# Kernel optimization log

Measured on AMD Instinct MI355X. Metric: run time of the kernel, lower is better.

Reference implementation:

```python
import jax, jax.numpy as jnp
import numpy as np

V = 100000   # vocab_size
E = 256      # embedding_dim
H = 256      # hidden_dim // 2 (per direction)
T = 32       # tagset_size
S = 4096     # seq_len
START, STOP = 30, 31
NEG = -10000.0


def setup_inputs() -> dict:
    key = jax.random.key(0)
    ks = jax.random.split(key, 13)
    sentence = jax.random.randint(ks[0], (S,), 0, V)
    h0 = jax.random.normal(ks[1], (2, H), dtype=jnp.float32)
    c0 = jax.random.normal(ks[2], (2, H), dtype=jnp.float32)
    embedding = jax.random.normal(ks[3], (V, E), dtype=jnp.float32) * 0.1
    # LSTM params, PyTorch layout: gates [i, f, g, o], combined bias = b_ih + b_hh
    w_ih_f = jax.random.normal(ks[4], (4 * H, E), dtype=jnp.float32) * 0.05
    w_hh_f = jax.random.normal(ks[5], (4 * H, H), dtype=jnp.float32) * 0.05
    b_f = jax.random.normal(ks[6], (4 * H,), dtype=jnp.float32) * 0.05
    w_ih_b = jax.random.normal(ks[7], (4 * H, E), dtype=jnp.float32) * 0.05
    w_hh_b = jax.random.normal(ks[8], (4 * H, H), dtype=jnp.float32) * 0.05
    b_b = jax.random.normal(ks[9], (4 * H,), dtype=jnp.float32) * 0.05
    lin_w = jax.random.normal(ks[10], (T, 2 * H), dtype=jnp.float32) * 0.05
    lin_b = jax.random.normal(ks[11], (T,), dtype=jnp.float32) * 0.05
    transitions = jax.random.normal(ks[12], (T, T), dtype=jnp.float32)
    transitions = transitions.at[START, :].set(NEG).at[:, STOP].set(NEG)
    return {"sentence": sentence, "h0": h0, "c0": c0, "embedding": embedding,
            "w_ih_f": w_ih_f, "w_hh_f": w_hh_f, "b_f": b_f,
            "w_ih_b": w_ih_b, "w_hh_b": w_hh_b, "b_b": b_b,
            "lin_w": lin_w, "lin_b": lin_b, "transitions": transitions}


def _lstm_dir(emb, h0, c0, w_ih, w_hh, b):
    # Precompute input contribution for all timesteps: [S, 4H]
    xg = emb @ w_ih.T + b

    def step(carry, xt):
        h, c = carry
        g = xt + h @ w_hh.T
        i, f, gg, o = jnp.split(g, 4)
        i = jax.nn.sigmoid(i); f = jax.nn.sigmoid(f)
        gg = jnp.tanh(gg); o = jax.nn.sigmoid(o)
        c = f * c + i * gg
        h = o * jnp.tanh(c)
        return (h, c), h

    _, hs = jax.lax.scan(step, (h0, c0), xg)
    return hs  # [S, H]


def reference(sentence, h0, c0, embedding, w_ih_f, w_hh_f, b_f,
              w_ih_b, w_hh_b, b_b, lin_w, lin_b, transitions):
    emb = embedding[sentence]                                    # [S, E]
    hs_f = _lstm_dir(emb, h0[0], c0[0], w_ih_f, w_hh_f, b_f)     # [S, H]
    hs_b = _lstm_dir(emb[::-1], h0[1], c0[1], w_ih_b, w_hh_b, b_b)[::-1]
    feats = jnp.concatenate([hs_f, hs_b], axis=-1) @ lin_w.T + lin_b  # [S, T]

    # Viterbi: forward_var over tags, vectorized over next/prev tags
    init = jnp.full((T,), NEG, dtype=feats.dtype).at[START].set(0.0)

    def vit_step(fv, feat):
        scores = fv[None, :] + transitions    # [next_tag, prev_tag]
        bp = jnp.argmax(scores, axis=1)       # best prev for each next tag
        fv_new = jnp.max(scores, axis=1) + feat
        return fv_new, bp

    fv, bps = jax.lax.scan(vit_step, init, feats)  # bps: [S, T]
    final = fv + transitions[STOP]
    last = jnp.argmax(final)
    score = final[last]

    # Backtrack (reverse scan); outputs[t] = best tag at timestep t
    def back_step(idx, bp):
        return bp[idx], idx

    _, path = jax.lax.scan(back_step, last, bps, reverse=True)
    return score, path
```

## Files before the change

### kernel.cpp

```cpp
#include <hip/hip_runtime.h>
#include <cstdint>
#include <cstddef>

#define S 4096
#define E 256
#define H 256
#define T 32
#define START_TAG 30
#define STOP_TAG 31
#define NEGV (-10000.0f)

typedef _Float16 half_t;
typedef _Float16 h2 __attribute__((ext_vector_type(2)));

__device__ __forceinline__ h2 f2h2(float a, float b) {
    h2 r; r[0] = (half_t)a; r[1] = (half_t)b; return r;
}
__device__ __forceinline__ h2 u2h2(unsigned int u) {
    h2 r; __builtin_memcpy(&r, &u, 4); return r;
}
__device__ __forceinline__ unsigned int h22u(h2 v) {
    unsigned int u; __builtin_memcpy(&u, &v, 4); return u;
}
__device__ __forceinline__ unsigned short f2h16(float f) {
    half_t h = (half_t)f;
    unsigned short u; __builtin_memcpy(&u, &h, 2); return u;
}
__device__ __forceinline__ float h16tof(unsigned short u) {
    half_t h; __builtin_memcpy(&h, &u, 2); return (float)h;
}

#if __has_builtin(__builtin_amdgcn_fdot2)
__device__ __forceinline__ float dot2(h2 a, h2 b, float c) {
    return __builtin_amdgcn_fdot2(a, b, c, false);
}
#else
__device__ __forceinline__ float dot2(h2 a, h2 b, float c) {
    return c + (float)a[0] * (float)b[0] + (float)a[1] * (float)b[1];
}
#endif

__device__ __forceinline__ float sigmoidf_(float x) {
    return 1.0f / (1.0f + __expf(-x));
}
__device__ __forceinline__ float tanhf_(float x) {
    return 1.0f - 2.0f / (__expf(2.0f * x) + 1.0f);
}

__device__ __forceinline__ float dpp_xor1_add(float x) {
    int yi = __builtin_amdgcn_update_dpp(0, __float_as_int(x), 0xB1, 0xF, 0xF, true);
    return x + __int_as_float(yi);
}

#define SBLK 16
__global__ __launch_bounds__(256) void xg_kernel(
    const int* __restrict__ sent, const float* __restrict__ emb,
    const float* __restrict__ w_ih_f, const float* __restrict__ b_f,
    const float* __restrict__ w_ih_b, const float* __restrict__ b_b,
    unsigned short* __restrict__ xg16s)
{
    const int dir = blockIdx.y;
    const int t0 = blockIdx.x * SBLK;
    const float* w_ih = dir ? w_ih_b : w_ih_f;
    const float* bias = dir ? b_b : b_f;

    __shared__ float embs[SBLK][E];
    for (int p = threadIdx.x; p < SBLK * (E / 4); p += 256) {
        int r = p >> 6, kq = p & 63;
        int t = t0 + r;
        int tt = dir ? (S - 1 - t) : t;
        int tok = sent[tt];
        float4 v = *(const float4*)(emb + (size_t)tok * E + 4 * kq);
        *(float4*)&embs[r][4 * kq] = v;
    }
    __syncthreads();

    for (int jj = 0; jj < 4; ++jj) {
        int j = jj * 256 + threadIdx.x;
        const float* wrow = w_ih + (size_t)j * E;
        float bv = bias[j];
        float acc[SBLK];
        #pragma unroll
        for (int t = 0; t < SBLK; ++t) acc[t] = bv;

        for (int kc = 0; kc < E / 16; ++kc) {
            float w[16];
            float4 a0 = *(const float4*)(wrow + kc * 16);
            float4 a1 = *(const float4*)(wrow + kc * 16 + 4);
            float4 a2 = *(const float4*)(wrow + kc * 16 + 8);
            float4 a3 = *(const float4*)(wrow + kc * 16 + 12);
            w[0] = a0.x; w[1] = a0.y; w[2] = a0.z; w[3] = a0.w;
            w[4] = a1.x; w[5] = a1.y; w[6] = a1.z; w[7] = a1.w;
            w[8] = a2.x; w[9] = a2.y; w[10] = a2.z; w[11] = a2.w;
            w[12] = a3.x; w[13] = a3.y; w[14] = a3.z; w[15] = a3.w;
            #pragma unroll
            for (int t = 0; t < SBLK; ++t) {
                const float* er = &embs[t][kc * 16];
                float s = 0.f;
                #pragma unroll
                for (int q = 0; q < 16; ++q) s += w[q] * er[q];
                acc[t] += s;
            }
        }
        const int u = threadIdx.x;
        #pragma unroll
        for (int t = 0; t < SBLK; ++t) {
            size_t base = (((size_t)dir * S + (size_t)(t0 + t)) * 256 + u) * 4 + jj;
            xg16s[base] = f2h16(acc[t]);
        }
    }
}

#define WL4_ENT 12
#define WL4_BYTES (WL4_ENT * 512 * 16)
#define LSTM_LDS_BYTES (WL4_BYTES + 2 * 128 * 4)

__global__ __launch_bounds__(512, 2) void lstm_kernel(
    const float* __restrict__ h0, const float* __restrict__ c0,
    const float* __restrict__ w_hh_f, const float* __restrict__ w_hh_b,
    const unsigned long long* __restrict__ xgq, float* __restrict__ hs)
{
    extern __shared__ char smem[];
    uint4* wl4 = (uint4*)smem;
    unsigned int* hbuf = (unsigned int*)(smem + WL4_BYTES);

    const int dir = blockIdx.x;
    const int tid = threadIdx.x;
    const int g = tid >> 1;
    const int p = tid & 1;
    const float* w_hh = dir ? w_hh_b : w_hh_f;

    const int rows[4] = { g, 256 + g, 512 + g, 768 + g };

    h2 wrI[52], wrF[52], wrG[52], wrO[52];
    {
        #pragma unroll
        for (int r = 0; r < 4; ++r) {
            const float* pr = w_hh + (size_t)rows[r] * H + p * 128;
            h2* dst = (r == 0) ? wrI : (r == 1) ? wrF : (r == 2) ? wrG : wrO;
            #pragma unroll
            for (int q2 = 0; q2 < 26; ++q2) {
                float4 a = *(const float4*)(pr + 4 * q2);
                dst[2 * q2]     = f2h2(a.x, a.y);
                dst[2 * q2 + 1] = f2h2(a.z, a.w);
            }
            #pragma unroll
            for (int lc = 0; lc < 3; ++lc) {
                float4 a = *(const float4*)(pr + 104 + 8 * lc);
                float4 b = *(const float4*)(pr + 108 + 8 * lc);
                uint4 w;
                w.x = h22u(f2h2(a.x, a.y));
                w.y = h22u(f2h2(a.z, a.w));
                w.z = h22u(f2h2(b.x, b.y));
                w.w = h22u(f2h2(b.z, b.w));
                wl4[(r * 3 + lc) * 512 + tid] = w;
            }
        }
    }

    float c = c0[dir * H + g];
    if (tid < 128) {
        float2 u = *(const float2*)(h0 + dir * H + 2 * tid);
        hbuf[tid] = h22u(f2h2(u.x, u.y));
    }
    __syncthreads();

    const unsigned long long* xgp = xgq + (size_t)dir * S * 256 + g;
    unsigned long long xgw = xgp[0];

    for (int t = 0; t < S; ++t) {
        int tn = (t + 1 < S) ? (t + 1) : t;
        unsigned long long xgn = xgp[(size_t)tn * 256];

        const int rbuf = t & 1;
        const uint4* hb4 = (const uint4*)(hbuf + rbuf * 128) + p * 16;

        float a0 = 0.f, a1 = 0.f, a2 = 0.f, a3 = 0.f;

        #pragma unroll
        for (int cc = 0; cc < 13; ++cc) {
            uint4 hv = hb4[cc];
            h2 hh0 = u2h2(hv.x), hh1 = u2h2(hv.y), hh2 = u2h2(hv.z), hh3 = u2h2(hv.w);
            a0 = dot2(wrI[cc * 4 + 0], hh0, a0);
            a0 = dot2(wrI[cc * 4 + 1], hh1, a0);
            a0 = dot2(wrI[cc * 4 + 2], hh2, a0);
            a0 = dot2(wrI[cc * 4 + 3], hh3, a0);
            a1 = dot2(wrF[cc * 4 + 0], hh0, a1);
            a1 = dot2(wrF[cc * 4 + 1], hh1, a1);
            a1 = dot2(wrF[cc * 4 + 2], hh2, a1);
            a1 = dot2(wrF[cc * 4 + 3], hh3, a1);
            a2 = dot2(wrG[cc * 4 + 0], hh0, a2);
            a2 = dot2(wrG[cc * 4 + 1], hh1, a2);
            a2 = dot2(wrG[cc * 4 + 2], hh2, a2);
            a2 = dot2(wrG[cc * 4 + 3], hh3, a2);
            a3 = dot2(wrO[cc * 4 + 0], hh0, a3);
            a3 = dot2(wrO[cc * 4 + 1], hh1, a3);
            a3 = dot2(wrO[cc * 4 + 2], hh2, a3);
            a3 = dot2(wrO[cc * 4 + 3], hh3, a3);
        }
        #pragma unroll
        for (int lc = 0; lc < 3; ++lc) {
            uint4 hv = hb4[13 + lc];
            h2 hh0 = u2h2(hv.x), hh1 = u2h2(hv.y), hh2 = u2h2(hv.z), hh3 = u2h2(hv.w);
            uint4 wI = wl4[(0 * 3 + lc) * 512 + tid];
            uint4 wF = wl4[(1 * 3 + lc) * 512 + tid];
            uint4 wG = wl4[(2 * 3 + lc) * 512 + tid];
            uint4 wO = wl4[(3 * 3 + lc) * 512 + tid];
            a0 = dot2(u2h2(wI.x), hh0, a0);
            a0 = dot2(u2h2(wI.y), hh1, a0);
            a0 = dot2(u2h2(wI.z), hh2, a0);
            a0 = dot2(u2h2(wI.w), hh3, a0);
            a1 = dot2(u2h2(wF.x), hh0, a1);
            a1 = dot2(u2h2(wF.y), hh1, a1);
            a1 = dot2(u2h2(wF.z), hh2, a1);
            a1 = dot2(u2h2(wF.w), hh3, a1);
            a2 = dot2(u2h2(wG.x), hh0, a2);
            a2 = dot2(u2h2(wG.y), hh1, a2);
            a2 = dot2(u2h2(wG.z), hh2, a2);
            a2 = dot2(u2h2(wG.w), hh3, a2);
            a3 = dot2(u2h2(wO.x), hh0, a3);
            a3 = dot2(u2h2(wO.y), hh1, a3);
            a3 = dot2(u2h2(wO.z), hh2, a3);
            a3 = dot2(u2h2(wO.w), hh3, a3);
        }

        float si = dpp_xor1_add(a0);
        float sf = dpp_xor1_add(a1);
        float sg = dpp_xor1_add(a2);
        float so = dpp_xor1_add(a3);

        unsigned int lo = (unsigned int)xgw;
        unsigned int hi = (unsigned int)(xgw >> 32);
        float gi = h16tof((unsigned short)(lo & 0xffffu)) + si;
        float gf = h16tof((unsigned short)(lo >> 16)) + sf;
        float gg = h16tof((unsigned short)(hi & 0xffffu)) + sg;
        float go = h16tof((unsigned short)(hi >> 16)) + so;

        float iv = sigmoidf_(gi);
        float fv = sigmoidf_(gf);
        float gv = tanhf_(gg);
        float ov = sigmoidf_(go);
        c = fv * c + iv * gv;
        float hv = ov * tanhf_(c);

        if (p == 0) {
            int row = dir ? (S - 1 - t) : t;
            hs[(size_t)row * 512 + dir * 256 + g] = hv;
            ((unsigned short*)(hbuf + ((t + 1) & 1) * 128))[g] = f2h16(hv);
        }
        xgw = xgn;
        __syncthreads();
    }
}

__global__ __launch_bounds__(256) void feats_kernel(
    const float* __restrict__ hs, const float* __restrict__ lin_w,
    const float* __restrict__ lin_b, float* __restrict__ feats)
{
    const int t0 = blockIdx.x * 8;
    __shared__ float rows[8][512];
    for (int p = threadIdx.x; p < 8 * 128; p += 256) {
        int r = p >> 7, sg = p & 127;
        float4 v = *(const float4*)(hs + (size_t)(t0 + r) * 512 + sg * 4);
        *(float4*)&rows[r][sg * 4] = v;
    }
    __syncthreads();

    const int tl = threadIdx.x >> 5, tag = threadIdx.x & 31;
    const float* lw = lin_w + (size_t)tag * 512;
    float acc = lin_b[tag];
    for (int kc = 0; kc < 32; ++kc) {
        float4 a0 = *(const float4*)(lw + kc * 16);
        float4 a1 = *(const float4*)(lw + kc * 16 + 4);
        float4 a2 = *(const float4*)(lw + kc * 16 + 8);
        float4 a3 = *(const float4*)(lw + kc * 16 + 12);
        const float* er = &rows[tl][kc * 16];
        acc += a0.x * er[0] + a0.y * er[1] + a0.z * er[2] + a0.w * er[3];
        acc += a1.x * er[4] + a1.y * er[5] + a1.z * er[6] + a1.w * er[7];
        acc += a2.x * er[8] + a2.y * er[9] + a2.z * er[10] + a2.w * er[11];
        acc += a3.x * er[12] + a3.y * er[13] + a3.z * er[14] + a3.w * er[15];
    }
    feats[(size_t)(t0 + tl) * T + tag] = acc;
}

#define VCS 64
#define VNC (S / VCS)
__global__ __launch_bounds__(256) void vit_chunk_kernel(
    const float* __restrict__ feats, const float* __restrict__ trans,
    float* __restrict__ gM)
{
    const int c = blockIdx.x;
    const int tid = threadIdx.x;
    const int n = tid >> 3, p0 = (tid & 7) * 4;
    __shared__ float Mb[2][32][36];

    float tr[32];
    #pragma unroll
    for (int k = 0; k < 32; ++k) tr[k] = trans[n * 32 + k];

    float f0 = feats[(size_t)(c * VCS) * 32 + n];
    float4 cur = { tr[p0] + f0, tr[p0 + 1] + f0, tr[p0 + 2] + f0, tr[p0 + 3] + f0 };
    *(float4*)&Mb[0][n][p0] = cur;
    __syncthreads();

    int rb = 0;
    for (int s = 1; s < VCS; ++s) {
        float fn = feats[(size_t)(c * VCS + s) * 32 + n];
        float4 acc = { -3.0e38f, -3.0e38f, -3.0e38f, -3.0e38f };
        #pragma unroll 8
        for (int k = 0; k < 32; ++k) {
            float4 mo = *(const float4*)&Mb[rb][k][p0];
            float tk = tr[k];
            acc.x = fmaxf(acc.x, tk + mo.x);
            acc.y = fmaxf(acc.y, tk + mo.y);
            acc.z = fmaxf(acc.z, tk + mo.z);
            acc.w = fmaxf(acc.w, tk + mo.w);
        }
        acc.x += fn; acc.y += fn; acc.z += fn; acc.w += fn;
        cur = acc;
        *(float4*)&Mb[rb ^ 1][n][p0] = acc;
        rb ^= 1;
        __syncthreads();
    }
    *(float4*)(gM + (size_t)c * 1024 + n * 32 + p0) = cur;
}

__global__ __launch_bounds__(1024) void vit_combine_kernel(
    const float* __restrict__ feats, const float* __restrict__ trans,
    const float* __restrict__ gM, unsigned char* __restrict__ gbp,
    float* __restrict__ out)
{
    __shared__ float MS[1024];
    __shared__ __align__(16) float bfv[VNC + 1][32];
    __shared__ __align__(16) float fvc[VNC][32];
    __shared__ unsigned char Mmap[VNC][32];
    __shared__ int ent[VNC];
    __shared__ int lastsh;

    const int tid = threadIdx.x;

    if (tid < 32) bfv[0][tid] = (tid == START_TAG) ? 0.f : NEGV;
    __syncthreads();
    for (int c = 0; c < VNC; ++c) {
        MS[tid] = gM[(size_t)c * 1024 + tid];
        __syncthreads();
        if (tid < 32) {
            float m = -3.0e38f;
            #pragma unroll 8
            for (int k = 0; k < 32; ++k)
                m = fmaxf(m, MS[tid * 32 + k] + bfv[c][k]);
            bfv[c + 1][tid] = m;
        }
        __syncthreads();
    }
    if (tid == 0) {
        float bm = -3.0e38f; int bl = 0;
        for (int j = 0; j < 32; ++j) {
            float s2 = bfv[VNC][j] + trans[STOP_TAG * 32 + j];
            if (s2 > bm) { bm = s2; bl = j; }
        }
        out[0] = bm;
        lastsh = bl;
    }
    __syncthreads();

    for (int pass = 0; pass < 2; ++pass) {
        const int c = (tid >> 5) + pass * 32;
        const int nt = tid & 31;
        float tr[32];
        #pragma unroll
        for (int k = 0; k < 32; ++k) tr[k] = trans[nt * 32 + k];

        fvc[c][nt] = bfv[c][nt];
        __builtin_amdgcn_wave_barrier();
        asm volatile("" ::: "memory");

        for (int s = 0; s < VCS; ++s) {
            const int t = c * VCS + s;
            float4 v0 = *(const float4*)&fvc[c][0];
            float4 v1 = *(const float4*)&fvc[c][4];
            float4 v2 = *(const float4*)&fvc[c][8];
            float4 v3 = *(const float4*)&fvc[c][12];
            float4 v4 = *(const float4*)&fvc[c][16];
            float4 v5 = *(const float4*)&fvc[c][20];
            float4 v6 = *(const float4*)&fvc[c][24];
            float4 v7 = *(const float4*)&fvc[c][28];
            float fvv[32] = { v0.x, v0.y, v0.z, v0.w, v1.x, v1.y, v1.z, v1.w,
                              v2.x, v2.y, v2.z, v2.w, v3.x, v3.y, v3.z, v3.w,
                              v4.x, v4.y, v4.z, v4.w, v5.x, v5.y, v5.z, v5.w,
                              v6.x, v6.y, v6.z, v6.w, v7.x, v7.y, v7.z, v7.w };
            float m = -3.0e38f; int bi = 0;
            #pragma unroll
            for (int k = 0; k < 32; ++k) {
                float s2 = fvv[k] + tr[k];
                if (s2 > m) { m = s2; bi = k; }
            }
            m += feats[(size_t)t * 32 + nt];
            gbp[(size_t)t * 32 + nt] = (unsigned char)bi;
            __builtin_amdgcn_wave_barrier();
            asm volatile("" ::: "memory");
            fvc[c][nt] = m;
            __builtin_amdgcn_wave_barrier();
            asm volatile("" ::: "memory");
        }
        __syncthreads();
    }

    {
        #pragma unroll
        for (int kk = 0; kk < 2; ++kk) {
            int it = tid + kk * 1024;
            int cc = it >> 5, st = it & 31;
            int cur = st;
            for (int s = VCS - 1; s >= 0; --s)
                cur = gbp[(size_t)(cc * VCS + s) * 32 + cur];
            Mmap[cc][st] = (unsigned char)cur;
        }
    }
    __syncthreads();

    if (tid == 0) {
        int cur = lastsh;
        ent[VNC - 1] = cur;
        for (int cchunk = VNC - 1; cchunk > 0; --cchunk) {
            cur = Mmap[cchunk][cur];
            ent[cchunk - 1] = cur;
        }
    }
    __syncthreads();

    if (tid < VNC) {
        int cur = ent[tid];
        for (int i = VCS - 1; i >= 0; --i) {
            int t = tid * VCS + i;
            out[1 + t] = (float)cur;
            cur = gbp[(size_t)t * 32 + cur];
        }
    }
}

extern "C" void kernel_launch(void* const* d_in, const int* in_sizes, int n_in,
                              void* d_out, int out_size, void* d_ws, size_t ws_size,
                              hipStream_t stream)
{
    const int* sent      = (const int*)d_in[0];
    const float* h0      = (const float*)d_in[1];
    const float* c0      = (const float*)d_in[2];
    const float* emb     = (const float*)d_in[3];
    const float* w_ih_f  = (const float*)d_in[4];
    const float* w_hh_f  = (const float*)d_in[5];
    const float* b_f     = (const float*)d_in[6];
    const float* w_ih_b  = (const float*)d_in[7];
    const float* w_hh_b  = (const float*)d_in[8];
    const float* b_b     = (const float*)d_in[9];
    const float* lin_w   = (const float*)d_in[10];
    const float* lin_b   = (const float*)d_in[11];
    const float* trans   = (const float*)d_in[12];
    float* out = (float*)d_out;

    unsigned long long* xgq = (unsigned long long*)d_ws;
    float* hs    = (float*)(xgq + (size_t)2 * S * 256);
    float* feats = hs + (size_t)S * 512;
    float* gM    = feats + (size_t)S * T;
    unsigned char* gbp = (unsigned char*)(gM + (size_t)VNC * 1024);

    hipFuncSetAttribute((const void*)lstm_kernel,
                        hipFuncAttributeMaxDynamicSharedMemorySize, LSTM_LDS_BYTES);

    xg_kernel<<<dim3(S / SBLK, 2), 256, 0, stream>>>(sent, emb, w_ih_f, b_f, w_ih_b, b_b,
                                                     (unsigned short*)xgq);
    lstm_kernel<<<2, 512, LSTM_LDS_BYTES, stream>>>(h0, c0, w_hh_f, w_hh_b, xgq, hs);
    feats_kernel<<<S / 8, 256, 0, stream>>>(hs, lin_w, lin_b, feats);
    vit_chunk_kernel<<<VNC, 256, 0, stream>>>(feats, trans, gM);
    vit_combine_kernel<<<1, 1024, 0, stream>>>(feats, trans, gM, gbp, out);
}
```

Before: 7.251 ms.

## Compute LSTM recurrent matvec with MFMA instructions and register-resident weights

Replaces the per-thread fdot2 recurrent matvec, which kept weights split between registers and LDS, with MFMA 16x16x32 f16 instructions. Each wave holds its full W_hh slice in registers as B operands, and the h vector is broadcast as the A operand. The input-gate contribution is folded into the accumulator initialisation, which removes the DPP reduction and the LDS weight reads. Most MFMA output lanes are wasted because only one row of h is real, and per-step latency now depends on MFMA dependency chains.

```diff
diff --git a/kernel.cpp b/kernel.cpp
--- a/kernel.cpp
+++ b/kernel.cpp
@@ -12,15 +12,11 @@
 
 typedef _Float16 half_t;
 typedef _Float16 h2 __attribute__((ext_vector_type(2)));
+typedef _Float16 f16x8 __attribute__((ext_vector_type(8)));
+typedef float f32x4 __attribute__((ext_vector_type(4)));
 
 __device__ __forceinline__ h2 f2h2(float a, float b) {
     h2 r; r[0] = (half_t)a; r[1] = (half_t)b; return r;
-}
-__device__ __forceinline__ h2 u2h2(unsigned int u) {
-    h2 r; __builtin_memcpy(&r, &u, 4); return r;
-}
-__device__ __forceinline__ unsigned int h22u(h2 v) {
-    unsigned int u; __builtin_memcpy(&u, &v, 4); return u;
 }
 __device__ __forceinline__ unsigned short f2h16(float f) {
     half_t h = (half_t)f;
@@ -30,16 +26,6 @@
     half_t h; __builtin_memcpy(&h, &u, 2); return (float)h;
 }
 
-#if __has_builtin(__builtin_amdgcn_fdot2)
-__device__ __forceinline__ float dot2(h2 a, h2 b, float c) {
-    return __builtin_amdgcn_fdot2(a, b, c, false);
-}
-#else
-__device__ __forceinline__ float dot2(h2 a, h2 b, float c) {
-    return c + (float)a[0] * (float)b[0] + (float)a[1] * (float)b[1];
-}
-#endif
-
 __device__ __forceinline__ float sigmoidf_(float x) {
     return 1.0f / (1.0f + __expf(-x));
 }
@@ -47,9 +33,11 @@
     return 1.0f - 2.0f / (__expf(2.0f * x) + 1.0f);
 }
 
-__device__ __forceinline__ float dpp_xor1_add(float x) {
-    int yi = __builtin_amdgcn_update_dpp(0, __float_as_int(x), 0xB1, 0xF, 0xF, true);
-    return x + __int_as_float(yi);
+__device__ __forceinline__ f16x8 cvt8(float4 a, float4 b) {
+    f16x8 v;
+    v[0] = (_Float16)a.x; v[1] = (_Float16)a.y; v[2] = (_Float16)a.z; v[3] = (_Float16)a.w;
+    v[4] = (_Float16)b.x; v[5] = (_Float16)b.y; v[6] = (_Float16)b.z; v[7] = (_Float16)b.w;
+    return v;
 }
 
 #define SBLK 16
@@ -111,142 +99,97 @@
     }
 }
 
-#define WL4_ENT 12
-#define WL4_BYTES (WL4_ENT * 512 * 16)
-#define LSTM_LDS_BYTES (WL4_BYTES + 2 * 128 * 4)
-
-__global__ __launch_bounds__(512, 2) void lstm_kernel(
+__global__ __launch_bounds__(512) void lstm_kernel(
     const float* __restrict__ h0, const float* __restrict__ c0,
     const float* __restrict__ w_hh_f, const float* __restrict__ w_hh_b,
     const unsigned long long* __restrict__ xgq, float* __restrict__ hs)
 {
-    extern __shared__ char smem[];
-    uint4* wl4 = (uint4*)smem;
-    unsigned int* hbuf = (unsigned int*)(smem + WL4_BYTES);
-
-    const int dir = blockIdx.x;
-    const int tid = threadIdx.x;
-    const int g = tid >> 1;
-    const int p = tid & 1;
+    __shared__ __align__(16) _Float16 hbuf[2][256];
+
+    const int dir  = blockIdx.x;
+    const int tid  = threadIdx.x;
+    const int lane = tid & 63;
+    const int w    = tid >> 6;
+    const int n    = lane & 15;
+    const int kg   = lane >> 4;
     const float* w_hh = dir ? w_hh_b : w_hh_f;
 
-    const int rows[4] = { g, 256 + g, 512 + g, 768 + g };
-
-    h2 wrI[52], wrF[52], wrG[52], wrO[52];
-    {
-        #pragma unroll
-        for (int r = 0; r < 4; ++r) {
-            const float* pr = w_hh + (size_t)rows[r] * H + p * 128;
-            h2* dst = (r == 0) ? wrI : (r == 1) ? wrF : (r == 2) ? wrG : wrO;
+    f16x8 wB[8][8];
+    #pragma unroll
+    for (int c = 0; c < 8; ++c) {
+        const int row = (c & 3) * 256 + w * 32 + 2 * n + (c >> 2);
+        const float* pr = w_hh + (size_t)row * H + kg * 8;
+        #pragma unroll
+        for (int kt = 0; kt < 8; ++kt) {
+            float4 a = *(const float4*)(pr + kt * 32);
+            float4 b = *(const float4*)(pr + kt * 32 + 4);
+            wB[c][kt] = cvt8(a, b);
+        }
+    }
+
+    const int  u_a    = w * 32 + 2 * n;
+    const bool hiU    = (kg >= 2);
+    const int  u_own  = u_a + (hiU ? 1 : 0);
+    const bool writer = (kg == 0) || (kg == 2);
+    float cst = c0[dir * H + u_own];
+
+    if (tid < 256) hbuf[0][tid] = (_Float16)h0[dir * H + tid];
+
+    const unsigned long long* xgl = xgq + (size_t)dir * S * 256 + u_a;
+    uint4 xgw = *(const uint4*)xgl;
+
+    __syncthreads();
+
+    for (int t = 0; t < S; ++t) {
+        const _Float16* hb = &hbuf[t & 1][0];
+        f16x8 hA[8];
+        #pragma unroll
+        for (int kt = 0; kt < 8; ++kt)
+            hA[kt] = *(const f16x8*)(hb + kt * 32 + kg * 8);
+
+        float xf[8];
+        xf[0] = h16tof((unsigned short)(xgw.x & 0xffffu));
+        xf[1] = h16tof((unsigned short)(xgw.x >> 16));
+        xf[2] = h16tof((unsigned short)(xgw.y & 0xffffu));
+        xf[3] = h16tof((unsigned short)(xgw.y >> 16));
+        xf[4] = h16tof((unsigned short)(xgw.z & 0xffffu));
+        xf[5] = h16tof((unsigned short)(xgw.z >> 16));
+        xf[6] = h16tof((unsigned short)(xgw.w & 0xffffu));
+        xf[7] = h16tof((unsigned short)(xgw.w >> 16));
+
+        f32x4 acc[8];
+        #pragma unroll
+        for (int c = 0; c < 8; ++c) {
+            f32x4 z = { xf[c], xf[c], xf[c], xf[c] };
+            acc[c] = z;
+        }
+
+        const int tn = (t + 1 < S) ? (t + 1) : t;
+        uint4 xgn = *(const uint4*)(xgl + (size_t)tn * 256);
+
+        #pragma unroll
+        for (int kt = 0; kt < 8; ++kt) {
             #pragma unroll
-            for (int q2 = 0; q2 < 26; ++q2) {
-                float4 a = *(const float4*)(pr + 4 * q2);
-                dst[2 * q2]     = f2h2(a.x, a.y);
-                dst[2 * q2 + 1] = f2h2(a.z, a.w);
-            }
-            #pragma unroll
-            for (int lc = 0; lc < 3; ++lc) {
-                float4 a = *(const float4*)(pr + 104 + 8 * lc);
-                float4 b = *(const float4*)(pr + 108 + 8 * lc);
-                uint4 w;
-                w.x = h22u(f2h2(a.x, a.y));
-                w.y = h22u(f2h2(a.z, a.w));
-                w.z = h22u(f2h2(b.x, b.y));
-                w.w = h22u(f2h2(b.z, b.w));
-                wl4[(r * 3 + lc) * 512 + tid] = w;
-            }
-        }
-    }
-
-    float c = c0[dir * H + g];
-    if (tid < 128) {
-        float2 u = *(const float2*)(h0 + dir * H + 2 * tid);
-        hbuf[tid] = h22u(f2h2(u.x, u.y));
-    }
-    __syncthreads();
-
-    const unsigned long long* xgp = xgq + (size_t)dir * S * 256 + g;
-    unsigned long long xgw = xgp[0];
-
-    for (int t = 0; t < S; ++t) {
-        int tn = (t + 1 < S) ? (t + 1) : t;
-        unsigned long long xgn = xgp[(size_t)tn * 256];
-
-        const int rbuf = t & 1;
-        const uint4* hb4 = (const uint4*)(hbuf + rbuf * 128) + p * 16;
-
-        float a0 = 0.f, a1 = 0.f, a2 = 0.f, a3 = 0.f;
-
-        #pragma unroll
-        for (int cc = 0; cc < 13; ++cc) {
-            uint4 hv = hb4[cc];
-            h2 hh0 = u2h2(hv.x), hh1 = u2h2(hv.y), hh2 = u2h2(hv.z), hh3 = u2h2(hv.w);
-            a0 = dot2(wrI[cc * 4 + 0], hh0, a0);
-            a0 = dot2(wrI[cc * 4 + 1], hh1, a0);
-            a0 = dot2(wrI[cc * 4 + 2], hh2, a0);
-            a0 = dot2(wrI[cc * 4 + 3], hh3, a0);
-            a1 = dot2(wrF[cc * 4 + 0], hh0, a1);
-            a1 = dot2(wrF[cc * 4 + 1], hh1, a1);
-            a1 = dot2(wrF[cc * 4 + 2], hh2, a1);
-            a1 = dot2(wrF[cc * 4 + 3], hh3, a1);
-            a2 = dot2(wrG[cc * 4 + 0], hh0, a2);
-            a2 = dot2(wrG[cc * 4 + 1], hh1, a2);
-            a2 = dot2(wrG[cc * 4 + 2], hh2, a2);
-            a2 = dot2(wrG[cc * 4 + 3], hh3, a2);
-            a3 = dot2(wrO[cc * 4 + 0], hh0, a3);
-            a3 = dot2(wrO[cc * 4 + 1], hh1, a3);
-            a3 = dot2(wrO[cc * 4 + 2], hh2, a3);
-            a3 = dot2(wrO[cc * 4 + 3], hh3, a3);
-        }
-        #pragma unroll
-        for (int lc = 0; lc < 3; ++lc) {
-            uint4 hv = hb4[13 + lc];
-            h2 hh0 = u2h2(hv.x), hh1 = u2h2(hv.y), hh2 = u2h2(hv.z), hh3 = u2h2(hv.w);
-            uint4 wI = wl4[(0 * 3 + lc) * 512 + tid];
-            uint4 wF = wl4[(1 * 3 + lc) * 512 + tid];
-            uint4 wG = wl4[(2 * 3 + lc) * 512 + tid];
-            uint4 wO = wl4[(3 * 3 + lc) * 512 + tid];
-            a0 = dot2(u2h2(wI.x), hh0, a0);
-            a0 = dot2(u2h2(wI.y), hh1, a0);
-            a0 = dot2(u2h2(wI.z), hh2, a0);
-            a0 = dot2(u2h2(wI.w), hh3, a0);
-            a1 = dot2(u2h2(wF.x), hh0, a1);
-            a1 = dot2(u2h2(wF.y), hh1, a1);
-            a1 = dot2(u2h2(wF.z), hh2, a1);
-            a1 = dot2(u2h2(wF.w), hh3, a1);
-            a2 = dot2(u2h2(wG.x), hh0, a2);
-            a2 = dot2(u2h2(wG.y), hh1, a2);
-            a2 = dot2(u2h2(wG.z), hh2, a2);
-            a2 = dot2(u2h2(wG.w), hh3, a2);
-            a3 = dot2(u2h2(wO.x), hh0, a3);
-            a3 = dot2(u2h2(wO.y), hh1, a3);
-            a3 = dot2(u2h2(wO.z), hh2, a3);
-            a3 = dot2(u2h2(wO.w), hh3, a3);
-        }
-
-        float si = dpp_xor1_add(a0);
-        float sf = dpp_xor1_add(a1);
-        float sg = dpp_xor1_add(a2);
-        float so = dpp_xor1_add(a3);
-
-        unsigned int lo = (unsigned int)xgw;
-        unsigned int hi = (unsigned int)(xgw >> 32);
-        float gi = h16tof((unsigned short)(lo & 0xffffu)) + si;
-        float gf = h16tof((unsigned short)(lo >> 16)) + sf;
-        float gg = h16tof((unsigned short)(hi & 0xffffu)) + sg;
-        float go = h16tof((unsigned short)(hi >> 16)) + so;
+            for (int c = 0; c < 8; ++c)
+                acc[c] = __builtin_amdgcn_mfma_f32_16x16x32_f16(hA[kt], wB[c][kt], acc[c], 0, 0, 0);
+        }
+
+        float gi = hiU ? acc[4][0] : acc[0][0];
+        float gf = hiU ? acc[5][0] : acc[1][0];
+        float gg = hiU ? acc[6][0] : acc[2][0];
+        float go = hiU ? acc[7][0] : acc[3][0];
 
         float iv = sigmoidf_(gi);
         float fv = sigmoidf_(gf);
         float gv = tanhf_(gg);
         float ov = sigmoidf_(go);
-        c = fv * c + iv * gv;
-        float hv = ov * tanhf_(c);
-
-        if (p == 0) {
+        cst = fv * cst + iv * gv;
+        float hv = ov * tanhf_(cst);
+
+        if (writer) {
+            hbuf[(t + 1) & 1][u_own] = (_Float16)hv;
             int row = dir ? (S - 1 - t) : t;
-            hs[(size_t)row * 512 + dir * 256 + g] = hv;
-            ((unsigned short*)(hbuf + ((t + 1) & 1) * 128))[g] = f2h16(hv);
+            hs[(size_t)row * 512 + dir * 256 + u_own] = hv;
         }
         xgw = xgn;
         __syncthreads();
@@ -464,12 +407,9 @@
     float* gM    = feats + (size_t)S * T;
     unsigned char* gbp = (unsigned char*)(gM + (size_t)VNC * 1024);
 
-    hipFuncSetAttribute((const void*)lstm_kernel,
-                        hipFuncAttributeMaxDynamicSharedMemorySize, LSTM_LDS_BYTES);
-
     xg_kernel<<<dim3(S / SBLK, 2), 256, 0, stream>>>(sent, emb, w_ih_f, b_f, w_ih_b, b_b,
                                                      (unsigned short*)xgq);
-    lstm_kernel<<<2, 512, LSTM_LDS_BYTES, stream>>>(h0, c0, w_hh_f, w_hh_b, xgq, hs);
+    lstm_kernel<<<2, 512, 0, stream>>>(h0, c0, w_hh_f, w_hh_b, xgq, hs);
     feats_kernel<<<S / 8, 256, 0, stream>>>(hs, lin_w, lin_b, feats);
     vit_chunk_kernel<<<VNC, 256, 0, stream>>>(feats, trans, gM);
     vit_combine_kernel<<<1, 1024, 0, stream>>>(feats, trans, gM, gbp, out);
```

Measured after the change: 13.93 ms. 1.92x slower.
